# Kernel optimization log

Hardware: AMD Instinct MI355X
Metric: run time of the kernel (lower is better)

The kernel has to match this reference:

```python
import jax, jax.numpy as jnp
import numpy as np

EPS_POS = 0.65
EPS_NEG = 0.4
TAU = 0.03
TEMPERATURE = 0.07


def setup_inputs() -> dict:
    key = jax.random.key(0)
    k1, k2 = jax.random.split(key)
    N, H, W, C = 256, 14, 14, 512  # ResNet18 layer4 features (448x448 frame), pooled audio
    frame = jax.random.normal(k1, (N, H, W, C), dtype=jnp.float32)
    audio = jax.random.normal(k2, (N, C), dtype=jnp.float32)
    return {"frame": frame, "audio": audio}


def reference(frame, audio):
    # frame: [N, H, W, C] vision backbone features; audio: [N, C] pooled audio embedding
    N = frame.shape[0]
    f = frame * jax.lax.rsqrt(jnp.sum(frame * frame, axis=3, keepdims=True))  # l2_normalize axis=3
    a = audio * jax.lax.rsqrt(jnp.sum(audio * audio, axis=1, keepdims=True))  # l2_normalize axis=1

    # S_ii: per-sample spatial similarity map [N, 1, H, W]
    S_ii = jnp.einsum('nhwc,nc->nhw', f, a)[:, None, :, :]
    # S_ij: cross-batch similarity [N, K, H, W] (K == N)
    S_ij = jnp.einsum('nhwc,kc->nkhw', f, a)

    m_ip = jax.nn.sigmoid((S_ii - EPS_POS) / TAU)   # positive soft-mask
    neg = 1.0 - jax.nn.sigmoid((S_ii - EPS_NEG) / TAU)  # hard-negative soft-mask

    # Pi: masked mean of positive similarities -> [N, 1]
    Pi = jnp.sum(m_ip * S_ii, axis=(2, 3)) / jnp.sum(m_ip, axis=(2, 3))

    n_all = jax.nn.sigmoid((S_ij - EPS_POS) / TAU)
    mask = 1.0 - 100.0 * jnp.eye(N, dtype=frame.dtype)  # kill diagonal (self) pairs
    Ni_easy = (jnp.sum(n_all * S_ij, axis=(2, 3)) / jnp.sum(n_all, axis=(2, 3))) * mask  # [N, N]
    Ni_hard = jnp.sum(neg * S_ii, axis=(2, 3)) / jnp.sum(neg, axis=(2, 3))  # [N, 1]

    data = jnp.concatenate([Pi, Ni_hard, Ni_easy], axis=1) * TEMPERATURE  # [N, N+2]

    # __calc_loss (faithful to TF broadcasting: Pi_d is [N,1], Ni_d is [N] -> [N,N] broadcast)
    Pi_d = data[:, 0:1]
    Ni_d = jnp.sum(data[:, 1:], axis=1)
    Pi_e = jnp.exp(Pi_d)
    Ni_e = jnp.exp(Ni_d)
    loss = (-1.0 / N) * jnp.sum(jnp.log(Pi_e / (Pi_e + Ni_e)))
    return loss
```

## Files before the change

kernel.cpp:

```cpp
#include <hip/hip_runtime.h>
#include <stdint.h>

#define NFR 256
#define HW 196
#define CH 512
#define EPS_POS 0.65f
#define EPS_NEG 0.40f
#define INV_TAU (1.0f/0.03f)
#define TEMP 0.07f

typedef __bf16 bf16x8 __attribute__((ext_vector_type(8)));
typedef float f32x4 __attribute__((ext_vector_type(4)));

typedef const __attribute__((address_space(1))) unsigned int* as1_u32p;
typedef __attribute__((address_space(3))) unsigned int* as3_u32p;
#define GLL(gp, lp) __builtin_amdgcn_global_load_lds((as1_u32p)(const void*)(gp), (as3_u32p)(void*)(lp), 16, 0, 0)

__device__ __forceinline__ float sigmoidf_(float x) {
  return 1.0f / (1.0f + __expf(-x));
}

__device__ __forceinline__ unsigned short f2bf(float x) {
  unsigned int u = __float_as_uint(x);
  unsigned int r = u + 0x7FFFu + ((u >> 16) & 1u);
  return (unsigned short)(r >> 16);
}

__global__ __launch_bounds__(64) void audio_norm_k(const float* __restrict__ audio,
                                                   unsigned short* __restrict__ abf) {
  const int r = blockIdx.x;
  const int l = threadIdx.x;
  const float4* src = reinterpret_cast<const float4*>(audio + (size_t)r * CH);
  float4 a = src[l];
  float4 b = src[64 + l];
  float ss = a.x*a.x + a.y*a.y + a.z*a.z + a.w*a.w
           + b.x*b.x + b.y*b.y + b.z*b.z + b.w*b.w;
#pragma unroll
  for (int m = 1; m < 64; m <<= 1) ss += __shfl_xor(ss, m);
  float sc = rsqrtf(ss);
  ushort4 o;
  o.x = f2bf(a.x*sc); o.y = f2bf(a.y*sc); o.z = f2bf(a.z*sc); o.w = f2bf(a.w*sc);
  reinterpret_cast<ushort4*>(abf + (size_t)r * CH)[l] = o;
  o.x = f2bf(b.x*sc); o.y = f2bf(b.y*sc); o.z = f2bf(b.z*sc); o.w = f2bf(b.w*sc);
  reinterpret_cast<ushort4*>(abf + (size_t)r * CH)[64 + l] = o;
}

__global__ __launch_bounds__(256) void frame_norm_k(const float* __restrict__ frame,
                                                    unsigned short* __restrict__ fbf) {
  const int w = threadIdx.x >> 6;
  const int l = threadIdx.x & 63;
  const size_t r = (size_t)blockIdx.x * 4 + w;
  const float4* src = reinterpret_cast<const float4*>(frame + r * CH);
  float4 a = src[l];
  float4 b = src[64 + l];
  float ss = a.x*a.x + a.y*a.y + a.z*a.z + a.w*a.w
           + b.x*b.x + b.y*b.y + b.z*b.z + b.w*b.w;
#pragma unroll
  for (int m = 1; m < 64; m <<= 1) ss += __shfl_xor(ss, m);
  float sc = rsqrtf(ss);
  ushort4 o;
  o.x = f2bf(a.x*sc); o.y = f2bf(a.y*sc); o.z = f2bf(a.z*sc); o.w = f2bf(a.w*sc);
  reinterpret_cast<ushort4*>(fbf + r * CH)[l] = o;
  o.x = f2bf(b.x*sc); o.y = f2bf(b.y*sc); o.z = f2bf(b.z*sc); o.w = f2bf(b.w*sc);
  reinterpret_cast<ushort4*>(fbf + r * CH)[64 + l] = o;
}

__global__ __launch_bounds__(256, 2) void simk(const unsigned short* __restrict__ fbf,
                                               const unsigned short* __restrict__ abf,
                                               float* __restrict__ num, float* __restrict__ den,
                                               float* __restrict__ negnum, float* __restrict__ negden) {
  __shared__ unsigned short Alds[2][128][32];
  __shared__ unsigned short Blds[2][128][32];
  const int tid = threadIdx.x;
  const int l = tid & 63, w = tid >> 6;
  const int wm = w >> 1, wn = w & 1;

  const int bid = blockIdx.x;
  const int vid = (bid & 7) * 98 + (bid >> 3);
  const int mt = vid >> 1;
  const int nt = vid & 1;
  const int m0 = mt * 128;
  const int n0col = nt * 128;

  const int srow = w * 16 + (l >> 2);
  const int scol = (l & 3) * 8;
  const unsigned short* agA = fbf + (size_t)(m0 + srow) * CH + scol;
  const unsigned short* agB = abf + (size_t)(n0col + srow) * CH + scol;

  GLL(agA,          &Alds[0][w * 16][0]);
  GLL(agA + 64*CH,  &Alds[0][64 + w * 16][0]);
  GLL(agB,          &Blds[0][w * 16][0]);
  GLL(agB + 64*CH,  &Blds[0][64 + w * 16][0]);
  __syncthreads();

  f32x4 acc[4][4] = {};
  const int rA0 = wm * 64 + (l & 15);
  const int rB0 = wn * 64 + (l & 15);
  const int kg8 = (l >> 4) * 8;
  int buf = 0;

  for (int t = 0; t < 16; ++t) {
    if (t < 15) {
      const unsigned short* a2 = agA + (t + 1) * 32;
      const unsigned short* b2 = agB + (t + 1) * 32;
      GLL(a2,          &Alds[buf ^ 1][w * 16][0]);
      GLL(a2 + 64*CH,  &Alds[buf ^ 1][64 + w * 16][0]);
      GLL(b2,          &Blds[buf ^ 1][w * 16][0]);
      GLL(b2 + 64*CH,  &Blds[buf ^ 1][64 + w * 16][0]);
    }
    bf16x8 af[4], bfr[4];
#pragma unroll
    for (int i = 0; i < 4; ++i) {
      af[i]  = *reinterpret_cast<const bf16x8*>(&Alds[buf][rA0 + i * 16][kg8]);
      bfr[i] = *reinterpret_cast<const bf16x8*>(&Blds[buf][rB0 + i * 16][kg8]);
    }
#pragma unroll
    for (int i = 0; i < 4; ++i)
#pragma unroll
      for (int j2 = 0; j2 < 4; ++j2)
        acc[i][j2] = __builtin_amdgcn_mfma_f32_16x16x32_bf16(af[i], bfr[j2], acc[i][j2], 0, 0, 0);
    __syncthreads();
    buf ^= 1;
  }

  const int rg = l >> 4;
  const int colL = l & 15;
  const int wrow0 = m0 + wm * 64;
  const int nlo = wrow0 / HW;
  const int nhi = (wrow0 + 63) / HW;

  float cn0[4] = {}, cd0[4] = {}, cn1[4] = {}, cd1[4] = {};
  float ngn = 0.f, ngd = 0.f;
  bool hasneg = false;
#pragma unroll
  for (int i = 0; i < 4; ++i) {
#pragma unroll
    for (int jj = 0; jj < 4; ++jj) {
      const int P = wrow0 + i * 16 + rg * 4 + jj;
      const int nrow = P / HW;
      const bool lo = (nrow == nlo);
#pragma unroll
      for (int j2 = 0; j2 < 4; ++j2) {
        const float s = acc[i][j2][jj];
        const float wp = sigmoidf_((s - EPS_POS) * INV_TAU);
        const float wps = wp * s;
        if (lo) { cn0[j2] += wps; cd0[j2] += wp; }
        else    { cn1[j2] += wps; cd1[j2] += wp; }
        const int kglob = n0col + wn * 64 + j2 * 16 + colL;
        if (kglob == nrow) {
          const float wneg = 1.f - sigmoidf_((s - EPS_NEG) * INV_TAU);
          ngn += wneg * s; ngd += wneg; hasneg = true;
        }
      }
    }
  }
  if (hasneg) { atomicAdd(&negnum[nlo == nhi ? nlo : (colL + n0col + wn*64 >= 0 ? 0 : 0), 0] , 0.f); }
  if (hasneg) {
  }

#pragma unroll
  for (int j2 = 0; j2 < 4; ++j2) {
    float v0 = cn0[j2], d0 = cd0[j2], v1 = cn1[j2], d1 = cd1[j2];
    v0 += __shfl_xor(v0, 16); v0 += __shfl_xor(v0, 32);
    d0 += __shfl_xor(d0, 16); d0 += __shfl_xor(d0, 32);
    v1 += __shfl_xor(v1, 16); v1 += __shfl_xor(v1, 32);
    d1 += __shfl_xor(d1, 16); d1 += __shfl_xor(d1, 32);
    if (rg == 0) {
      const int kglob = n0col + wn * 64 + j2 * 16 + colL;
      atomicAdd(&num[nlo * NFR + kglob], v0);
      atomicAdd(&den[nlo * NFR + kglob], d0);
      if (nhi != nlo) {
        atomicAdd(&num[nhi * NFR + kglob], v1);
        atomicAdd(&den[nhi * NFR + kglob], d1);
      }
    }
  }
  if (hasneg) {
    float gn0 = 0.f, gd0 = 0.f, gn1 = 0.f, gd1 = 0.f;
#pragma unroll
    for (int i = 0; i < 4; ++i) {
#pragma unroll
      for (int jj = 0; jj < 4; ++jj) {
        const int P = wrow0 + i * 16 + rg * 4 + jj;
        const int nrow = P / HW;
#pragma unroll
        for (int j2 = 0; j2 < 4; ++j2) {
          const int kglob = n0col + wn * 64 + j2 * 16 + colL;
          if (kglob == nrow) {
            const float s = acc[i][j2][jj];
            const float wneg = 1.f - sigmoidf_((s - EPS_NEG) * INV_TAU);
            if (nrow == nlo) { gn0 += wneg * s; gd0 += wneg; }
            else             { gn1 += wneg * s; gd1 += wneg; }
          }
        }
      }
    }
    if (gd0 > 0.f) { atomicAdd(&negnum[nlo], gn0); atomicAdd(&negden[nlo], gd0); }
    if (gd1 > 0.f) { atomicAdd(&negnum[nhi], gn1); atomicAdd(&negden[nhi], gd1); }
  }
}

__global__ __launch_bounds__(64) void rowstats_k(const float* __restrict__ num,
                                                 const float* __restrict__ den,
                                                 const float* __restrict__ negnum,
                                                 const float* __restrict__ negden,
                                                 float* __restrict__ Pi_d,
                                                 float* __restrict__ Ni_d) {
  const int r = blockIdx.x;
  const int l = threadIdx.x;
  float vsum = 0.f, pvac = 0.f;
#pragma unroll
  for (int cb = 0; cb < 4; ++cb) {
    const int k = cb * 64 + l;
    const float ratio = num[r * NFR + k] / den[r * NFR + k];
    vsum += ratio;
    if (k == r) pvac = ratio;
  }
#pragma unroll
  for (int m = 1; m < 64; m <<= 1) {
    vsum += __shfl_xor(vsum, m);
    pvac += __shfl_xor(pvac, m);
  }
  if (l == 0) {
    const float nh = negnum[r] / negden[r];
    Pi_d[r] = TEMP * pvac;
    Ni_d[r] = TEMP * (nh + vsum - 100.f * pvac);
  }
}

__global__ __launch_bounds__(256) void loss_k(const float* __restrict__ Pi_d,
                                              const float* __restrict__ Ni_d,
                                              float* __restrict__ out) {
  __shared__ float red[4];
  const int i = blockIdx.x;
  const int tid = threadIdx.x;
  const int l = tid & 63, w = tid >> 6;
  const float x = Ni_d[tid] - Pi_d[i];
  const float m = fmaxf(x, 0.f);
  float sp = m + __logf(__expf(x - m) + __expf(-m));
#pragma unroll
  for (int s2 = 1; s2 < 64; s2 <<= 1) sp += __shfl_xor(sp, s2);
  if (l == 0) red[w] = sp;
  __syncthreads();
  if (tid == 0) atomicAdd(out, (red[0] + red[1] + red[2] + red[3]) * (1.0f / (float)NFR));
}

extern "C" void kernel_launch(void* const* d_in, const int* in_sizes, int n_in,
                              void* d_out, int out_size, void* d_ws, size_t ws_size,
                              hipStream_t stream) {
  const float* frame = (const float*)d_in[0];
  const float* audio = (const float*)d_in[1];
  float* out = (float*)d_out;

  char* ws = (char*)d_ws;
  unsigned short* abf = (unsigned short*)ws;
  unsigned short* fbf = (unsigned short*)(ws + 262144);
  float* num    = (float*)(ws + 262144 + 51380224);
  float* den    = num + NFR * NFR;
  float* negnum = den + NFR * NFR;
  float* negden = negnum + NFR;
  float* Pi_d   = negden + NFR;
  float* Ni_d   = Pi_d + NFR;

  hipMemsetAsync(num, 0, (size_t)(2 * NFR * NFR + 2 * NFR) * sizeof(float), stream);
  hipMemsetAsync(out, 0, sizeof(float), stream);

  audio_norm_k<<<256, 64, 0, stream>>>(audio, abf);
  frame_norm_k<<<12544, 256, 0, stream>>>(frame, fbf);
  simk<<<784, 256, 0, stream>>>(fbf, abf, num, den, negnum, negden);
  rowstats_k<<<256, 64, 0, stream>>>(num, den, negnum, negden, Pi_d, Ni_d);
  loss_k<<<256, 256, 0, stream>>>(Pi_d, Ni_d, out);
}
```

Measured before the change: 216.9 us.

## Retile similarity GEMM to 64x256 blocks with swizzled LDS and fused negative pass

Each block now computes 64 frame rows against all 256 audio columns, so each of the four waves owns a 64-column slice and every frame row is loaded from global memory once. The LDS column index is XOR-swizzled on both the async load and the fragment reads to avoid bank conflicts. The hard-negative accumulation now happens in the first epilogue pass, which removes the second sweep over the accumulators and a leftover dummy atomic. Occupancy is hinted to three blocks per CU; the trade-offs are more audio traffic into LDS per block, since the full B matrix is loaded each time, and a different register and LDS footprint.

```diff
diff --git a/kernel.cpp b/kernel.cpp
--- a/kernel.cpp
+++ b/kernel.cpp
@@ -65,108 +65,98 @@
   reinterpret_cast<ushort4*>(fbf + r * CH)[64 + l] = o;
 }
 
-__global__ __launch_bounds__(256, 2) void simk(const unsigned short* __restrict__ fbf,
+__global__ __launch_bounds__(256, 3) void simk(const unsigned short* __restrict__ fbf,
                                                const unsigned short* __restrict__ abf,
                                                float* __restrict__ num, float* __restrict__ den,
                                                float* __restrict__ negnum, float* __restrict__ negden) {
-  __shared__ unsigned short Alds[2][128][32];
-  __shared__ unsigned short Blds[2][128][32];
+  __shared__ unsigned short Alds[2][64][32];
+  __shared__ unsigned short Blds[2][256][32];
   const int tid = threadIdx.x;
   const int l = tid & 63, w = tid >> 6;
-  const int wm = w >> 1, wn = w & 1;
-
-  const int bid = blockIdx.x;
-  const int vid = (bid & 7) * 98 + (bid >> 3);
-  const int mt = vid >> 1;
-  const int nt = vid & 1;
-  const int m0 = mt * 128;
-  const int n0col = nt * 128;
-
-  const int srow = w * 16 + (l >> 2);
-  const int scol = (l & 3) * 8;
-  const unsigned short* agA = fbf + (size_t)(m0 + srow) * CH + scol;
-  const unsigned short* agB = abf + (size_t)(n0col + srow) * CH + scol;
-
-  GLL(agA,          &Alds[0][w * 16][0]);
-  GLL(agA + 64*CH,  &Alds[0][64 + w * 16][0]);
-  GLL(agB,          &Blds[0][w * 16][0]);
-  GLL(agB + 64*CH,  &Blds[0][64 + w * 16][0]);
+  const int m0 = blockIdx.x * 64;
+
+  const int scol = (((l & 3) ^ ((l >> 3) & 3)) * 8);
+  const unsigned short* agA = fbf + (size_t)(m0 + 16 * w + (l >> 2)) * CH + scol;
+  const unsigned short* agB = abf + (size_t)(64 * w + (l >> 2)) * CH + scol;
+
+  GLL(agA, &Alds[0][16 * w][0]);
+#pragma unroll
+  for (int q = 0; q < 4; ++q)
+    GLL(agB + (size_t)(16 * q) * CH, &Blds[0][64 * w + 16 * q][0]);
   __syncthreads();
 
   f32x4 acc[4][4] = {};
-  const int rA0 = wm * 64 + (l & 15);
-  const int rB0 = wn * 64 + (l & 15);
-  const int kg8 = (l >> 4) * 8;
+  const int rA = l & 15;
+  const int cswz = (((l >> 4) ^ ((l >> 1) & 3)) << 4);
   int buf = 0;
 
   for (int t = 0; t < 16; ++t) {
     if (t < 15) {
-      const unsigned short* a2 = agA + (t + 1) * 32;
-      const unsigned short* b2 = agB + (t + 1) * 32;
-      GLL(a2,          &Alds[buf ^ 1][w * 16][0]);
-      GLL(a2 + 64*CH,  &Alds[buf ^ 1][64 + w * 16][0]);
-      GLL(b2,          &Blds[buf ^ 1][w * 16][0]);
-      GLL(b2 + 64*CH,  &Blds[buf ^ 1][64 + w * 16][0]);
-    }
+      const int ko = (t + 1) * 32;
+      GLL(agA + ko, &Alds[buf ^ 1][16 * w][0]);
+#pragma unroll
+      for (int q = 0; q < 4; ++q)
+        GLL(agB + ko + (size_t)(16 * q) * CH, &Blds[buf ^ 1][64 * w + 16 * q][0]);
+    }
+    const char* Ab = (const char*)&Alds[buf][0][0] + rA * 64 + cswz;
+    const char* Bb = (const char*)&Blds[buf][0][0] + (64 * w + rA) * 64 + cswz;
     bf16x8 af[4], bfr[4];
 #pragma unroll
     for (int i = 0; i < 4; ++i) {
-      af[i]  = *reinterpret_cast<const bf16x8*>(&Alds[buf][rA0 + i * 16][kg8]);
-      bfr[i] = *reinterpret_cast<const bf16x8*>(&Blds[buf][rB0 + i * 16][kg8]);
+      af[i]  = *reinterpret_cast<const bf16x8*>(Ab + 1024 * i);
+      bfr[i] = *reinterpret_cast<const bf16x8*>(Bb + 1024 * i);
     }
 #pragma unroll
     for (int i = 0; i < 4; ++i)
 #pragma unroll
-      for (int j2 = 0; j2 < 4; ++j2)
-        acc[i][j2] = __builtin_amdgcn_mfma_f32_16x16x32_bf16(af[i], bfr[j2], acc[i][j2], 0, 0, 0);
+      for (int j = 0; j < 4; ++j)
+        acc[i][j] = __builtin_amdgcn_mfma_f32_16x16x32_bf16(af[i], bfr[j], acc[i][j], 0, 0, 0);
     __syncthreads();
     buf ^= 1;
   }
 
   const int rg = l >> 4;
   const int colL = l & 15;
-  const int wrow0 = m0 + wm * 64;
-  const int nlo = wrow0 / HW;
-  const int nhi = (wrow0 + 63) / HW;
+  const int nlo = m0 / HW;
+  const int nhi = (m0 + 63) / HW;
 
   float cn0[4] = {}, cd0[4] = {}, cn1[4] = {}, cd1[4] = {};
-  float ngn = 0.f, ngd = 0.f;
-  bool hasneg = false;
+  float gn0 = 0.f, gd0 = 0.f, gn1 = 0.f, gd1 = 0.f;
 #pragma unroll
   for (int i = 0; i < 4; ++i) {
 #pragma unroll
     for (int jj = 0; jj < 4; ++jj) {
-      const int P = wrow0 + i * 16 + rg * 4 + jj;
+      const int P = m0 + i * 16 + rg * 4 + jj;
       const int nrow = P / HW;
       const bool lo = (nrow == nlo);
 #pragma unroll
-      for (int j2 = 0; j2 < 4; ++j2) {
-        const float s = acc[i][j2][jj];
+      for (int j = 0; j < 4; ++j) {
+        const float s = acc[i][j][jj];
         const float wp = sigmoidf_((s - EPS_POS) * INV_TAU);
         const float wps = wp * s;
-        if (lo) { cn0[j2] += wps; cd0[j2] += wp; }
-        else    { cn1[j2] += wps; cd1[j2] += wp; }
-        const int kglob = n0col + wn * 64 + j2 * 16 + colL;
+        if (lo) { cn0[j] += wps; cd0[j] += wp; }
+        else    { cn1[j] += wps; cd1[j] += wp; }
+        const int kglob = w * 64 + j * 16 + colL;
         if (kglob == nrow) {
           const float wneg = 1.f - sigmoidf_((s - EPS_NEG) * INV_TAU);
-          ngn += wneg * s; ngd += wneg; hasneg = true;
+          if (lo) { gn0 += wneg * s; gd0 += wneg; }
+          else    { gn1 += wneg * s; gd1 += wneg; }
         }
       }
     }
   }
-  if (hasneg) { atomicAdd(&negnum[nlo == nhi ? nlo : (colL + n0col + wn*64 >= 0 ? 0 : 0), 0] , 0.f); }
-  if (hasneg) {
-  }
-
-#pragma unroll
-  for (int j2 = 0; j2 < 4; ++j2) {
-    float v0 = cn0[j2], d0 = cd0[j2], v1 = cn1[j2], d1 = cd1[j2];
+  if (gd0 > 0.f) { atomicAdd(&negnum[nlo], gn0); atomicAdd(&negden[nlo], gd0); }
+  if (gd1 > 0.f) { atomicAdd(&negnum[nhi], gn1); atomicAdd(&negden[nhi], gd1); }
+
+#pragma unroll
+  for (int j = 0; j < 4; ++j) {
+    float v0 = cn0[j], d0 = cd0[j], v1 = cn1[j], d1 = cd1[j];
     v0 += __shfl_xor(v0, 16); v0 += __shfl_xor(v0, 32);
     d0 += __shfl_xor(d0, 16); d0 += __shfl_xor(d0, 32);
     v1 += __shfl_xor(v1, 16); v1 += __shfl_xor(v1, 32);
     d1 += __shfl_xor(d1, 16); d1 += __shfl_xor(d1, 32);
     if (rg == 0) {
-      const int kglob = n0col + wn * 64 + j2 * 16 + colL;
+      const int kglob = w * 64 + j * 16 + colL;
       atomicAdd(&num[nlo * NFR + kglob], v0);
       atomicAdd(&den[nlo * NFR + kglob], d0);
       if (nhi != nlo) {
@@ -174,29 +164,6 @@
         atomicAdd(&den[nhi * NFR + kglob], d1);
       }
     }
-  }
-  if (hasneg) {
-    float gn0 = 0.f, gd0 = 0.f, gn1 = 0.f, gd1 = 0.f;
-#pragma unroll
-    for (int i = 0; i < 4; ++i) {
-#pragma unroll
-      for (int jj = 0; jj < 4; ++jj) {
-        const int P = wrow0 + i * 16 + rg * 4 + jj;
-        const int nrow = P / HW;
-#pragma unroll
-        for (int j2 = 0; j2 < 4; ++j2) {
-          const int kglob = n0col + wn * 64 + j2 * 16 + colL;
-          if (kglob == nrow) {
-            const float s = acc[i][j2][jj];
-            const float wneg = 1.f - sigmoidf_((s - EPS_NEG) * INV_TAU);
-            if (nrow == nlo) { gn0 += wneg * s; gd0 += wneg; }
-            else             { gn1 += wneg * s; gd1 += wneg; }
-          }
-        }
-      }
-    }
-    if (gd0 > 0.f) { atomicAdd(&negnum[nlo], gn0); atomicAdd(&negden[nlo], gd0); }
-    if (gd1 > 0.f) { atomicAdd(&negnum[nhi], gn1); atomicAdd(&negden[nhi], gd1); }
   }
 }
 
```

After: 202.6 us. -6.6%, faster.
